# Performance work log

Hardware: AMD Instinct MI355X
Metric: run time of the kernel (lower is better)

## Reference

```python
import jax, jax.numpy as jnp
import numpy as np

EMBED_DIM = 768
NUM_HEADS = 12
HEAD_DIM = EMBED_DIM // NUM_HEADS
SCALE = HEAD_DIM ** -0.5


def setup_inputs() -> dict:
    key = jax.random.key(0)
    ks = jax.random.split(key, 9)
    B, S, D = 2, 2048, EMBED_DIM
    init = 1.0 / np.sqrt(D)  # ~ nn.Linear default uniform scale
    x = jax.random.normal(ks[0], (B, S, D), dtype=jnp.float32)
    Wq = jax.random.uniform(ks[1], (D, D), jnp.float32, -init, init)
    bq = jax.random.uniform(ks[2], (D,), jnp.float32, -init, init)
    Wk = jax.random.uniform(ks[3], (D, D), jnp.float32, -init, init)
    bk = jax.random.uniform(ks[4], (D,), jnp.float32, -init, init)
    Wv = jax.random.uniform(ks[5], (D, D), jnp.float32, -init, init)
    bv = jax.random.uniform(ks[6], (D,), jnp.float32, -init, init)
    Wo = jax.random.uniform(ks[7], (D, D), jnp.float32, -init, init)
    bo = jax.random.uniform(ks[8], (D,), jnp.float32, -init, init)
    return {"x": x, "Wq": Wq, "bq": bq, "Wk": Wk, "bk": bk,
            "Wv": Wv, "bv": bv, "Wo": Wo, "bo": bo}


def reference(x, Wq, bq, Wk, bk, Wv, bv, Wo, bo):
    B, S, D = x.shape
    H, Dh = NUM_HEADS, HEAD_DIM
    # projections; weights stored as (in, out) so x @ W == torch Linear with W.T
    q = (x @ Wq + bq).reshape(B, S, H, Dh).transpose(0, 2, 1, 3)  # [B,H,S,Dh]
    k = (x @ Wk + bk).reshape(B, S, H, Dh).transpose(0, 2, 1, 3)
    v = (x @ Wv + bv).reshape(B, S, H, Dh).transpose(0, 2, 1, 3)
    scores = jnp.einsum("bhqd,bhkd->bhqk", q, k) * SCALE        # [B,H,S,S]
    weights = jax.nn.softmax(scores, axis=-1)
    out = jnp.einsum("bhqk,bhkd->bhqd", weights, v)              # [B,H,S,Dh]
    out = out.transpose(0, 2, 1, 3).reshape(B, S, D)
    return out @ Wo + bo
```

## Files before the change

### kernel.cpp

```cpp
#include <hip/hip_runtime.h>
#include <math.h>

#define BB 2
#define SS 2048
#define DDIM 768
#define HH 12
#define DH 64
#define NROWS (BB*SS)
#define NQT2 (SS/128)
#define NSPLIT 4

typedef _Float16 f16;
typedef _Float16 half2v __attribute__((ext_vector_type(2)));
typedef __fp16 fp16x2 __attribute__((ext_vector_type(2)));
typedef _Float16 half4 __attribute__((ext_vector_type(4)));
typedef _Float16 half8 __attribute__((ext_vector_type(8)));
typedef float f32x4 __attribute__((ext_vector_type(4)));
typedef float f32x16 __attribute__((ext_vector_type(16)));
typedef unsigned int u32;
typedef unsigned int u32x4v __attribute__((ext_vector_type(4)));

__device__ __forceinline__ half2v cvt_pk_f16(float a, float b) {
    fp16x2 t = __builtin_amdgcn_cvt_pkrtz(a, b);
    return __builtin_bit_cast(half2v, t);
}

#define MFMA16(a,b,c) __builtin_amdgcn_mfma_f32_16x16x32_f16((a),(b),(c),0,0,0)
#define MFMA32(a,b,c) __builtin_amdgcn_mfma_f32_32x32x16_f16((a),(b),(c),0,0,0)
#define QSCALE (0.125f * 1.44269504088896f)
#define M_STATIC 10.0f

__device__ __forceinline__ int swz(int row, int chunk16) {
    return row*128 + ((chunk16 ^ (row & 7)) << 4);
}

__global__ __launch_bounds__(256) void prep_w(const float* __restrict__ Wq, const float* __restrict__ Wk,
                                              const float* __restrict__ Wv, const float* __restrict__ Wo,
                                              f16* __restrict__ Wt)
{
    const int z = blockIdx.z;
    const float* W = z==0 ? Wq : (z==1 ? Wk : (z==2 ? Wv : Wo));
    f16* out = Wt + (size_t)z * DDIM * DDIM;

    __shared__ float tile[64][65];
    const int t = threadIdx.x;
    const int k0 = blockIdx.x*64, n0 = blockIdx.y*64;

    const int kr = t >> 2, nc = (t & 3) * 16;
    #pragma unroll
    for (int i = 0; i < 4; ++i) {
        float4 v = *(const float4*)&W[(size_t)(k0+kr)*DDIM + n0 + nc + i*4];
        tile[kr][nc+i*4+0] = v.x; tile[kr][nc+i*4+1] = v.y;
        tile[kr][nc+i*4+2] = v.z; tile[kr][nc+i*4+3] = v.w;
    }
    __syncthreads();
    const int nr = t >> 2, kc = (t & 3) * 16;
    half8 h0, h1;
    #pragma unroll
    for (int j = 0; j < 8; ++j) {
        h0[j] = (f16)tile[kc + j][nr];
        h1[j] = (f16)tile[kc + 8 + j][nr];
    }
    *(half8*)&out[(size_t)(n0+nr)*DDIM + k0 + kc]     = h0;
    *(half8*)&out[(size_t)(n0+nr)*DDIM + k0 + kc + 8] = h1;
}

__global__ __launch_bounds__(256) void proj_qkv(const float* __restrict__ x, const f16* __restrict__ Wt,
        const float* __restrict__ bq, const float* __restrict__ bk, const float* __restrict__ bv,
        f16* __restrict__ qb, f16* __restrict__ kb2, f16* __restrict__ vtb)
{
    const int z = blockIdx.z;
    const f16* Wz = Wt + (size_t)z * DDIM * DDIM;
    const float* bias = z==0 ? bq : (z==1 ? bk : bv);
    const float qscale = (z==0) ? QSCALE : 1.0f;

    __shared__ __align__(16) unsigned char lds[64*1024];

    const int tid = threadIdx.x;
    const int l = tid & 63, w = tid >> 6;
    const int g = l >> 4, qi = l & 15;
    const int wm = w >> 1, wn = w & 1;
    const int m0 = blockIdx.x * 128, n0 = blockIdx.y * 128;

    f32x4 acc[4][4];
    #pragma unroll
    for (int i=0;i<4;i++)
        #pragma unroll
        for (int j=0;j<4;j++) { f32x4 zv = {0.f,0.f,0.f,0.f}; acc[i][j] = zv; }

    half8 sa[4], sb[4];

#define GLOAD(t) { \
        _Pragma("unroll") \
        for (int i = 0; i < 4; ++i) { \
            int c = i*256 + tid, row = c >> 3, kc = c & 7; \
            const float* xp = &x[(size_t)(m0+row)*DDIM + (t)*64 + kc*8]; \
            float4 a0 = *(const float4*)xp; \
            float4 a1 = *(const float4*)(xp + 4); \
            half8 hv = {(f16)a0.x,(f16)a0.y,(f16)a0.z,(f16)a0.w, \
                        (f16)a1.x,(f16)a1.y,(f16)a1.z,(f16)a1.w}; \
            sa[i] = hv; \
            sb[i] = *(const half8*)&Wz[(size_t)(n0+row)*DDIM + (t)*64 + kc*8]; \
        } }

#define GWRT(bufi) { \
        unsigned char* As_ = lds + (bufi)*32768; \
        unsigned char* Bs_ = As_ + 16384; \
        _Pragma("unroll") \
        for (int i = 0; i < 4; ++i) { \
            int c = i*256 + tid, row = c >> 3, kc = c & 7; \
            *(half8*)(As_ + swz(row, kc)) = sa[i]; \
            *(half8*)(Bs_ + swz(row, kc)) = sb[i]; \
        } }

    GLOAD(0); GWRT(0);
    __syncthreads();

    for (int t = 0; t < 12; ++t) {
        const int cur = t & 1;
        if (t < 11) GLOAD(t+1);

        const unsigned char* As = lds + cur*32768;
        const unsigned char* Bs = As + 16384;

        half8 af[4][2], bf[4][2];
        #pragma unroll
        for (int mt = 0; mt < 4; ++mt) {
            int row = wm*64 + mt*16 + qi;
            #pragma unroll
            for (int kh = 0; kh < 2; ++kh)
                af[mt][kh] = *(const half8*)(As + swz(row, kh*4 + g));
        }
        #pragma unroll
        for (int nt = 0; nt < 4; ++nt) {
            int row = wn*64 + nt*16 + qi;
            #pragma unroll
            for (int kh = 0; kh < 2; ++kh)
                bf[nt][kh] = *(const half8*)(Bs + swz(row, kh*4 + g));
        }
        __builtin_amdgcn_s_setprio(1);
        #pragma unroll
        for (int mt = 0; mt < 4; ++mt)
            #pragma unroll
            for (int nt = 0; nt < 4; ++nt) {
                acc[mt][nt] = MFMA16(af[mt][0], bf[nt][0], acc[mt][nt]);
                acc[mt][nt] = MFMA16(af[mt][1], bf[nt][1], acc[mt][nt]);
            }
        __builtin_amdgcn_s_setprio(0);

        if (t < 11) GWRT(cur^1);
        __syncthreads();
    }

    if (z == 2) {
        #pragma unroll
        for (int mt = 0; mt < 4; ++mt)
            #pragma unroll
            for (int nt = 0; nt < 4; ++nt) {
                int m = m0 + wm*64 + mt*16 + g*4;
                int n = n0 + wn*64 + nt*16 + qi;
                int b = m >> 11, s = m & 2047;
                int h = n >> 6,  d = n & 63;
                float bs = bias[n];
                half4 o4 = {(f16)(acc[mt][nt][0] + bs), (f16)(acc[mt][nt][1] + bs),
                            (f16)(acc[mt][nt][2] + bs), (f16)(acc[mt][nt][3] + bs)};
                *(half4*)&vtb[(((size_t)(b*HH + h))*DH + d)*SS + s] = o4;
            }
    } else {
        f16* out = (z == 0) ? qb : kb2;
        #pragma unroll
        for (int mt = 0; mt < 4; ++mt)
            #pragma unroll
            for (int nt = 0; nt < 4; ++nt)
                #pragma unroll
                for (int r = 0; r < 4; ++r) {
                    int m = m0 + wm*64 + mt*16 + g*4 + r;
                    int n = n0 + wn*64 + nt*16 + qi;
                    float v = (acc[mt][nt][r] + bias[n]) * qscale;
                    int b = m >> 11, s = m & 2047;
                    int h = n >> 6,  d = n & 63;
                    out[(((size_t)(b*HH + h))*SS + s)*DH + d] = (f16)v;
                }
    }
#undef GLOAD
#undef GWRT
}

__global__ __launch_bounds__(256) void attn_mfma(
        const f16* __restrict__ qbuf, const f16* __restrict__ kbuf,
        const f16* __restrict__ vtbuf, f16* __restrict__ pO, float* __restrict__ mlb)
{
    __shared__ __align__(16) unsigned char lds[32*1024];

    const int tid = threadIdx.x;
    const int l = tid & 63, w = tid >> 6;
    const int q31 = l & 31, hl = l >> 5;
    const int qt = blockIdx.x, h = blockIdx.y;
    const int b = blockIdx.z >> 2, kq = blockIdx.z & 3;
    const int q0 = qt * 128 + w * 32;
    const size_t base = ((size_t)(b * HH + h)) * SS * DH;
    const int key0 = kq * (SS/NSPLIT);
    const int pid = (b * HH + h) * NQT2 + qt;

    half8 qf[4];
    #pragma unroll
    for (int s = 0; s < 4; ++s)
        qf[s] = *(const half8*)&qbuf[base + (size_t)(q0 + q31)*DH + s*16 + hl*8];

    f32x16 oacc[2];
    #pragma unroll
    for (int dt = 0; dt < 2; ++dt)
        #pragma unroll
        for (int i = 0; i < 16; ++i) oacc[dt][i] = 0.f;
    float lsum = 0.f;
    f32x16 minit16;
    #pragma unroll
    for (int i = 0; i < 16; ++i) minit16[i] = -M_STATIC;

    half8 sk[2], svv[2];

#define LOADT(t) { \
        _Pragma("unroll") \
        for (int i = 0; i < 2; ++i) { \
            int c = i*256 + tid, row = c >> 3, col = c & 7; \
            sk[i]  = *(const half8*)&kbuf[base + (size_t)(key0 + (t)*64 + row)*DH + col*8]; \
            svv[i] = *(const half8*)&vtbuf[base + (size_t)row*SS + key0 + (t)*64 + col*8]; \
        } }

#define WRT(bufi) { \
        unsigned char* Kw_ = lds + (bufi)*16384; \
        unsigned char* Vw_ = Kw_ + 8192; \
        _Pragma("unroll") \
        for (int i = 0; i < 2; ++i) { \
            int c = i*256 + tid, row = c >> 3, col = c & 7; \
            *(half8*)(Kw_ + swz(row, col)) = sk[i]; \
            *(half8*)(Vw_ + swz(row, col)) = svv[i]; \
        } }

    LOADT(0); WRT(0);
    __syncthreads();

    for (int t = 0; t < 8; ++t) {
        const int cur = t & 1;
        if (t < 7) LOADT(t+1);

        const unsigned char* Kb = lds + cur*16384;
        const unsigned char* Vb = Kb + 8192;

        half8 kA[2][4];
        #pragma unroll
        for (int mt = 0; mt < 2; ++mt)
            #pragma unroll
            for (int s = 0; s < 4; ++s)
                kA[mt][s] = *(const half8*)(Kb + swz(mt*32 + q31, 2*s + hl));
        half8 vA[2][4];
        #pragma unroll
        for (int dt = 0; dt < 2; ++dt)
            #pragma unroll
            for (int ks = 0; ks < 4; ++ks)
                vA[dt][ks] = *(const half8*)(Vb + swz(dt*32 + q31, 2*ks + hl));

        half2v ph[16];
        #pragma unroll
        for (int mt = 0; mt < 2; ++mt) {
            __builtin_amdgcn_s_setprio(1);
            f32x16 sv = minit16;
            #pragma unroll
            for (int s = 0; s < 4; ++s)
                sv = MFMA32(kA[mt][s], qf[s], sv);
            __builtin_amdgcn_s_setprio(0);
            #pragma unroll
            for (int r = 0; r < 16; r += 2)
                ph[mt*8 + (r>>1)] = cvt_pk_f16(exp2f(sv[r]), exp2f(sv[r+1]));
        }

        {
            half2v t01 = (ph[0]+ph[1]) + (ph[2]+ph[3]);
            half2v t23 = (ph[4]+ph[5]) + (ph[6]+ph[7]);
            half2v t45 = (ph[8]+ph[9]) + (ph[10]+ph[11]);
            half2v t67 = (ph[12]+ph[13]) + (ph[14]+ph[15]);
            half2v tt = (t01+t23) + (t45+t67);
            float rs = (float)tt[0] + (float)tt[1];
            rs += __shfl_xor(rs, 32);
            lsum += rs;
        }

        half8 pf[4];
        #pragma unroll
        for (int ks = 0; ks < 4; ++ks) {
            u32 x0 = __builtin_bit_cast(u32, ph[4*ks + 0]);
            u32 x2 = __builtin_bit_cast(u32, ph[4*ks + 2]);
            asm volatile("v_permlane32_swap_b32 %0, %1" : "+v"(x0), "+v"(x2));
            u32 x1 = __builtin_bit_cast(u32, ph[4*ks + 1]);
            u32 x3 = __builtin_bit_cast(u32, ph[4*ks + 3]);
            asm volatile("v_permlane32_swap_b32 %0, %1" : "+v"(x1), "+v"(x3));
            u32x4v tv = {x0, x1, x2, x3};
            pf[ks] = __builtin_bit_cast(half8, tv);
        }

        __builtin_amdgcn_s_setprio(1);
        #pragma unroll
        for (int dt = 0; dt < 2; ++dt)
            #pragma unroll
            for (int ks = 0; ks < 4; ++ks)
                oacc[dt] = MFMA32(vA[dt][ks], pf[ks], oacc[dt]);
        __builtin_amdgcn_s_setprio(0);

        if (t < 7) WRT(cur^1);
        __syncthreads();
    }

    f16* po = pO + ((size_t)pid*NSPLIT + kq) * (128*64);
    float* mlp = mlb + ((size_t)pid*NSPLIT + kq) * 128;
    const int qw = w*32 + q31;
    const float inv = 1.0f / lsum;
    #pragma unroll
    for (int dt = 0; dt < 2; ++dt)
        #pragma unroll
        for (int g2 = 0; g2 < 4; ++g2) {
            half4 o4 = {(f16)(oacc[dt][g2*4+0]*inv), (f16)(oacc[dt][g2*4+1]*inv),
                        (f16)(oacc[dt][g2*4+2]*inv), (f16)(oacc[dt][g2*4+3]*inv)};
            *(half4*)&po[qw*64 + dt*32 + g2*8 + hl*4] = o4;
        }
    if (hl == 0) mlp[qw] = lsum;
#undef LOADT
#undef WRT
}

__global__ __launch_bounds__(256) void attn_combine(
        const f16* __restrict__ pO, const float* __restrict__ mlb, f16* __restrict__ ob)
{
    const int gr = blockIdx.x*64 + (threadIdx.x >> 2);
    const int dg = (threadIdx.x & 3) << 4;
    const int bh = gr >> 11, s = gr & 2047;
    const int qt = s >> 7, qr = s & 127;
    const int pid = bh * NQT2 + qt;

    float lv[NSPLIT], lt = 0.f;
    #pragma unroll
    for (int i = 0; i < NSPLIT; ++i) {
        lv[i] = mlb[((size_t)pid*NSPLIT + i)*128 + qr];
        lt += lv[i];
    }
    const float inv = 1.0f / lt;

    float a0[8] = {}, a1[8] = {};
    #pragma unroll
    for (int i = 0; i < NSPLIT; ++i) {
        const f16* Oi = pO + ((size_t)pid*NSPLIT + i)*(128*64) + qr*64 + dg;
        half8 x0 = *(const half8*)Oi;
        half8 x1 = *(const half8*)(Oi + 8);
        float wi = lv[i] * inv;
        #pragma unroll
        for (int j = 0; j < 8; ++j) {
            a0[j] += wi * (float)x0[j];
            a1[j] += wi * (float)x1[j];
        }
    }
    half8 r0, r1;
    #pragma unroll
    for (int j = 0; j < 8; ++j) { r0[j] = (f16)a0[j]; r1[j] = (f16)a1[j]; }
    f16* dst = &ob[((size_t)bh*SS + s)*DH + dg];
    *(half8*)dst = r0;
    *(half8*)(dst + 8) = r1;
}

__global__ __launch_bounds__(256) void proj_out(const f16* __restrict__ obuf, const f16* __restrict__ Wt,
                                                const float* __restrict__ bo, float* __restrict__ out)
{
    const f16* Wz = Wt + (size_t)3 * DDIM * DDIM;

    __shared__ __align__(16) unsigned char lds[64*1024];

    const int tid = threadIdx.x;
    const int l = tid & 63, w = tid >> 6;
    const int g = l >> 4, qi = l & 15;
    const int wm = w >> 1, wn = w & 1;
    const int m0 = blockIdx.x * 128, n0 = blockIdx.y * 128;

    f32x4 acc[4][4];
    #pragma unroll
    for (int i=0;i<4;i++)
        #pragma unroll
        for (int j=0;j<4;j++) { f32x4 zv = {0.f,0.f,0.f,0.f}; acc[i][j] = zv; }

    half8 sa[4], sb[4];

#define GLOAD(t) { \
        _Pragma("unroll") \
        for (int i = 0; i < 4; ++i) { \
            int c = i*256 + tid, row = c >> 3, kc = c & 7; \
            int m = m0 + row, bb_ = m >> 11, ss_ = m & 2047; \
            sa[i] = *(const half8*)&obuf[(((size_t)(bb_*HH + (t)))*SS + ss_)*DH + kc*8]; \
            sb[i] = *(const half8*)&Wz[(size_t)(n0+row)*DDIM + (t)*64 + kc*8]; \
        } }

#define GWRT(bufi) { \
        unsigned char* As_ = lds + (bufi)*32768; \
        unsigned char* Bs_ = As_ + 16384; \
        _Pragma("unroll") \
        for (int i = 0; i < 4; ++i) { \
            int c = i*256 + tid, row = c >> 3, kc = c & 7; \
            *(half8*)(As_ + swz(row, kc)) = sa[i]; \
            *(half8*)(Bs_ + swz(row, kc)) = sb[i]; \
        } }

    GLOAD(0); GWRT(0);
    __syncthreads();

    for (int t = 0; t < 12; ++t) {
        const int cur = t & 1;
        if (t < 11) GLOAD(t+1);

        const unsigned char* As = lds + cur*32768;
        const unsigned char* Bs = As + 16384;

        half8 af[4][2], bf[4][2];
        #pragma unroll
        for (int mt = 0; mt < 4; ++mt) {
            int row = wm*64 + mt*16 + qi;
            #pragma unroll
            for (int kh = 0; kh < 2; ++kh)
                af[mt][kh] = *(const half8*)(As + swz(row, kh*4 + g));
        }
        #pragma unroll
        for (int nt = 0; nt < 4; ++nt) {
            int row = wn*64 + nt*16 + qi;
            #pragma unroll
            for (int kh = 0; kh < 2; ++kh)
                bf[nt][kh] = *(const half8*)(Bs + swz(row, kh*4 + g));
        }
        __builtin_amdgcn_s_setprio(1);
        #pragma unroll
        for (int mt = 0; mt < 4; ++mt)
            #pragma unroll
            for (int nt = 0; nt < 4; ++nt) {
                acc[mt][nt] = MFMA16(af[mt][0], bf[nt][0], acc[mt][nt]);
                acc[mt][nt] = MFMA16(af[mt][1], bf[nt][1], acc[mt][nt]);
            }
        __builtin_amdgcn_s_setprio(0);

        if (t < 11) GWRT(cur^1);
        __syncthreads();
    }

    #pragma unroll
    for (int mt = 0; mt < 4; ++mt)
        #pragma unroll
        for (int nt = 0; nt < 4; ++nt)
            #pragma unroll
            for (int r = 0; r < 4; ++r) {
                int m = m0 + wm*64 + mt*16 + g*4 + r;
                int n = n0 + wn*64 + nt*16 + qi;
                out[(size_t)m*DDIM + n] = acc[mt][nt][r] + bo[n];
            }
#undef GLOAD
#undef GWRT
}

extern "C" void kernel_launch(void* const* d_in, const int* in_sizes, int n_in,
                              void* d_out, int out_size, void* d_ws, size_t ws_size,
                              hipStream_t stream)
{
    const float* x  = (const float*)d_in[0];
    const float* Wq = (const float*)d_in[1];
    const float* bq = (const float*)d_in[2];
    const float* Wk = (const float*)d_in[3];
    const float* bk = (const float*)d_in[4];
    const float* Wv = (const float*)d_in[5];
    const float* bv = (const float*)d_in[6];
    const float* Wo = (const float*)d_in[7];
    const float* bo = (const float*)d_in[8];

    char* ws = (char*)d_ws;
    const size_t WT_B  = (size_t)4 * DDIM * DDIM * 2;
    const size_t HB_B  = (size_t)BB * HH * SS * DH * 2;
    const size_t PO_B  = (size_t)BB * HH * NQT2 * NSPLIT * 128 * 64 * 2;
    const size_t ML_B  = (size_t)BB * HH * NQT2 * NSPLIT * 128 * 4;

    f16* Wt = (f16*)ws;
    f16* qb = (f16*)(ws + WT_B);
    f16* kb = (f16*)(ws + WT_B + HB_B);
    f16* vt = (f16*)(ws + WT_B + 2*HB_B);
    f16* pO = (f16*)(ws + WT_B + 3*HB_B);
    float* mlb = (float*)(ws + WT_B + 3*HB_B + PO_B);
    f16* ob = (f16*)(ws + WT_B + 3*HB_B + PO_B + ML_B);

    prep_w<<<dim3(DDIM/64, DDIM/64, 4), 256, 0, stream>>>(Wq, Wk, Wv, Wo, Wt);
    proj_qkv<<<dim3(NROWS/128, DDIM/128, 3), 256, 0, stream>>>(x, Wt, bq, bk, bv, qb, kb, vt);
    attn_mfma<<<dim3(NQT2, HH, BB*NSPLIT), 256, 0, stream>>>(qb, kb, vt, pO, mlb);
    attn_combine<<<dim3(BB*HH*SS/64), 256, 0, stream>>>(pO, mlb, ob);
    proj_out<<<dim3(NROWS/128, DDIM/128), 256, 0, stream>>>(ob, Wt, bo, (float*)d_out);
}
```

Measured before the change: 118.6 us.

## Shrink projection GEMM tiles to 64x128 with single-buffered LDS

```diff
diff --git a/kernel.cpp b/kernel.cpp
--- a/kernel.cpp
+++ b/kernel.cpp
@@ -74,25 +74,27 @@
     const float* bias = z==0 ? bq : (z==1 ? bk : bv);
     const float qscale = (z==0) ? QSCALE : 1.0f;
 
-    __shared__ __align__(16) unsigned char lds[64*1024];
+    __shared__ __align__(16) unsigned char lds[24*1024];
+    unsigned char* As = lds;
+    unsigned char* Bs = lds + 8192;
 
     const int tid = threadIdx.x;
     const int l = tid & 63, w = tid >> 6;
     const int g = l >> 4, qi = l & 15;
     const int wm = w >> 1, wn = w & 1;
-    const int m0 = blockIdx.x * 128, n0 = blockIdx.y * 128;
-
-    f32x4 acc[4][4];
-    #pragma unroll
-    for (int i=0;i<4;i++)
+    const int m0 = blockIdx.x * 64, n0 = blockIdx.y * 128;
+
+    f32x4 acc[2][4];
+    #pragma unroll
+    for (int i=0;i<2;i++)
         #pragma unroll
         for (int j=0;j<4;j++) { f32x4 zv = {0.f,0.f,0.f,0.f}; acc[i][j] = zv; }
 
-    half8 sa[4], sb[4];
+    half8 sa[2], sb[4];
 
 #define GLOAD(t) { \
         _Pragma("unroll") \
-        for (int i = 0; i < 4; ++i) { \
+        for (int i = 0; i < 2; ++i) { \
             int c = i*256 + tid, row = c >> 3, kc = c & 7; \
             const float* xp = &x[(size_t)(m0+row)*DDIM + (t)*64 + kc*8]; \
             float4 a0 = *(const float4*)xp; \
@@ -100,33 +102,35 @@
             half8 hv = {(f16)a0.x,(f16)a0.y,(f16)a0.z,(f16)a0.w, \
                         (f16)a1.x,(f16)a1.y,(f16)a1.z,(f16)a1.w}; \
             sa[i] = hv; \
+        } \
+        _Pragma("unroll") \
+        for (int i = 0; i < 4; ++i) { \
+            int c = i*256 + tid, row = c >> 3, kc = c & 7; \
             sb[i] = *(const half8*)&Wz[(size_t)(n0+row)*DDIM + (t)*64 + kc*8]; \
         } }
 
-#define GWRT(bufi) { \
-        unsigned char* As_ = lds + (bufi)*32768; \
-        unsigned char* Bs_ = As_ + 16384; \
+#define GWRT { \
+        _Pragma("unroll") \
+        for (int i = 0; i < 2; ++i) { \
+            int c = i*256 + tid, row = c >> 3, kc = c & 7; \
+            *(half8*)(As + swz(row, kc)) = sa[i]; \
+        } \
         _Pragma("unroll") \
         for (int i = 0; i < 4; ++i) { \
             int c = i*256 + tid, row = c >> 3, kc = c & 7; \
-            *(half8*)(As_ + swz(row, kc)) = sa[i]; \
-            *(half8*)(Bs_ + swz(row, kc)) = sb[i]; \
+            *(half8*)(Bs + swz(row, kc)) = sb[i]; \
         } }
 
-    GLOAD(0); GWRT(0);
+    GLOAD(0); GWRT;
     __syncthreads();
 
     for (int t = 0; t < 12; ++t) {
-        const int cur = t & 1;
         if (t < 11) GLOAD(t+1);
 
-        const unsigned char* As = lds + cur*32768;
-        const unsigned char* Bs = As + 16384;
-
-        half8 af[4][2], bf[4][2];
-        #pragma unroll
-        for (int mt = 0; mt < 4; ++mt) {
-            int row = wm*64 + mt*16 + qi;
+        half8 af[2][2], bf[4][2];
+        #pragma unroll
+        for (int mt = 0; mt < 2; ++mt) {
+            int row = wm*32 + mt*16 + qi;
             #pragma unroll
             for (int kh = 0; kh < 2; ++kh)
                 af[mt][kh] = *(const half8*)(As + swz(row, kh*4 + g));
@@ -140,7 +144,7 @@
         }
         __builtin_amdgcn_s_setprio(1);
         #pragma unroll
-        for (int mt = 0; mt < 4; ++mt)
+        for (int mt = 0; mt < 2; ++mt)
             #pragma unroll
             for (int nt = 0; nt < 4; ++nt) {
                 acc[mt][nt] = MFMA16(af[mt][0], bf[nt][0], acc[mt][nt]);
@@ -148,16 +152,19 @@
             }
         __builtin_amdgcn_s_setprio(0);
 
-        if (t < 11) GWRT(cur^1);
-        __syncthreads();
+        if (t < 11) {
+            __syncthreads();
+            GWRT;
+            __syncthreads();
+        }
     }
 
     if (z == 2) {
         #pragma unroll
-        for (int mt = 0; mt < 4; ++mt)
+        for (int mt = 0; mt < 2; ++mt)
             #pragma unroll
             for (int nt = 0; nt < 4; ++nt) {
-                int m = m0 + wm*64 + mt*16 + g*4;
+                int m = m0 + wm*32 + mt*16 + g*4;
                 int n = n0 + wn*64 + nt*16 + qi;
                 int b = m >> 11, s = m & 2047;
                 int h = n >> 6,  d = n & 63;
@@ -169,12 +176,12 @@
     } else {
         f16* out = (z == 0) ? qb : kb2;
         #pragma unroll
-        for (int mt = 0; mt < 4; ++mt)
+        for (int mt = 0; mt < 2; ++mt)
             #pragma unroll
             for (int nt = 0; nt < 4; ++nt)
                 #pragma unroll
                 for (int r = 0; r < 4; ++r) {
-                    int m = m0 + wm*64 + mt*16 + g*4 + r;
+                    int m = m0 + wm*32 + mt*16 + g*4 + r;
                     int n = n0 + wn*64 + nt*16 + qi;
                     float v = (acc[mt][nt][r] + bias[n]) * qscale;
                     int b = m >> 11, s = m & 2047;
@@ -370,55 +377,59 @@
 {
     const f16* Wz = Wt + (size_t)3 * DDIM * DDIM;
 
-    __shared__ __align__(16) unsigned char lds[64*1024];
+    __shared__ __align__(16) unsigned char lds[24*1024];
+    unsigned char* As = lds;
+    unsigned char* Bs = lds + 8192;
 
     const int tid = threadIdx.x;
     const int l = tid & 63, w = tid >> 6;
     const int g = l >> 4, qi = l & 15;
     const int wm = w >> 1, wn = w & 1;
-    const int m0 = blockIdx.x * 128, n0 = blockIdx.y * 128;
-
-    f32x4 acc[4][4];
-    #pragma unroll
-    for (int i=0;i<4;i++)
+    const int m0 = blockIdx.x * 64, n0 = blockIdx.y * 128;
+
+    f32x4 acc[2][4];
+    #pragma unroll
+    for (int i=0;i<2;i++)
         #pragma unroll
         for (int j=0;j<4;j++) { f32x4 zv = {0.f,0.f,0.f,0.f}; acc[i][j] = zv; }
 
-    half8 sa[4], sb[4];
+    half8 sa[2], sb[4];
 
 #define GLOAD(t) { \
         _Pragma("unroll") \
-        for (int i = 0; i < 4; ++i) { \
+        for (int i = 0; i < 2; ++i) { \
             int c = i*256 + tid, row = c >> 3, kc = c & 7; \
             int m = m0 + row, bb_ = m >> 11, ss_ = m & 2047; \
             sa[i] = *(const half8*)&obuf[(((size_t)(bb_*HH + (t)))*SS + ss_)*DH + kc*8]; \
+        } \
+        _Pragma("unroll") \
+        for (int i = 0; i < 4; ++i) { \
+            int c = i*256 + tid, row = c >> 3, kc = c & 7; \
             sb[i] = *(const half8*)&Wz[(size_t)(n0+row)*DDIM + (t)*64 + kc*8]; \
         } }
 
-#define GWRT(bufi) { \
-        unsigned char* As_ = lds + (bufi)*32768; \
-        unsigned char* Bs_ = As_ + 16384; \
+#define GWRT { \
+        _Pragma("unroll") \
+        for (int i = 0; i < 2; ++i) { \
+            int c = i*256 + tid, row = c >> 3, kc = c & 7; \
+            *(half8*)(As + swz(row, kc)) = sa[i]; \
+        } \
         _Pragma("unroll") \
         for (int i = 0; i < 4; ++i) { \
             int c = i*256 + tid, row = c >> 3, kc = c & 7; \
-            *(half8*)(As_ + swz(row, kc)) = sa[i]; \
-            *(half8*)(Bs_ + swz(row, kc)) = sb[i]; \
+            *(half8*)(Bs + swz(row, kc)) = sb[i]; \
         } }
 
-    GLOAD(0); GWRT(0);
+    GLOAD(0); GWRT;
     __syncthreads();
 
     for (int t = 0; t < 12; ++t) {
-        const int cur = t & 1;
         if (t < 11) GLOAD(t+1);
 
-        const unsigned char* As = lds + cur*32768;
-        const unsigned char* Bs = As + 16384;
-
-        half8 af[4][2], bf[4][2];
-        #pragma unroll
-        for (int mt = 0; mt < 4; ++mt) {
-            int row = wm*64 + mt*16 + qi;
+        half8 af[2][2], bf[4][2];
+        #pragma unroll
+        for (int mt = 0; mt < 2; ++mt) {
+            int row = wm*32 + mt*16 + qi;
             #pragma unroll
             for (int kh = 0; kh < 2; ++kh)
                 af[mt][kh] = *(const half8*)(As + swz(row, kh*4 + g));
@@ -432,7 +443,7 @@
         }
         __builtin_amdgcn_s_setprio(1);
         #pragma unroll
-        for (int mt = 0; mt < 4; ++mt)
+        for (int mt = 0; mt < 2; ++mt)
             #pragma unroll
             for (int nt = 0; nt < 4; ++nt) {
                 acc[mt][nt] = MFMA16(af[mt][0], bf[nt][0], acc[mt][nt]);
@@ -440,17 +451,20 @@
             }
         __builtin_amdgcn_s_setprio(0);
 
-        if (t < 11) GWRT(cur^1);
-        __syncthreads();
-    }
-
-    #pragma unroll
-    for (int mt = 0; mt < 4; ++mt)
+        if (t < 11) {
+            __syncthreads();
+            GWRT;
+            __syncthreads();
+        }
+    }
+
+    #pragma unroll
+    for (int mt = 0; mt < 2; ++mt)
         #pragma unroll
         for (int nt = 0; nt < 4; ++nt)
             #pragma unroll
             for (int r = 0; r < 4; ++r) {
-                int m = m0 + wm*64 + mt*16 + g*4 + r;
+                int m = m0 + wm*32 + mt*16 + g*4 + r;
                 int n = n0 + wn*64 + nt*16 + qi;
                 out[(size_t)m*DDIM + n] = acc[mt][nt][r] + bo[n];
             }
@@ -487,8 +501,8 @@
     f16* ob = (f16*)(ws + WT_B + 3*HB_B + PO_B + ML_B);
 
     prep_w<<<dim3(DDIM/64, DDIM/64, 4), 256, 0, stream>>>(Wq, Wk, Wv, Wo, Wt);
-    proj_qkv<<<dim3(NROWS/128, DDIM/128, 3), 256, 0, stream>>>(x, Wt, bq, bk, bv, qb, kb, vt);
+    proj_qkv<<<dim3(NROWS/64, DDIM/128, 3), 256, 0, stream>>>(x, Wt, bq, bk, bv, qb, kb, vt);
     attn_mfma<<<dim3(NQT2, HH, BB*NSPLIT), 256, 0, stream>>>(qb, kb, vt, pO, mlb);
     attn_combine<<<dim3(BB*HH*SS/64), 256, 0, stream>>>(pO, mlb, ob);
-    proj_out<<<dim3(NROWS/128, DDIM/128), 256, 0, stream>>>(ob, Wt, bo, (float*)d_out);
-}
+    proj_out<<<dim3(NROWS/64, DDIM/128), 256, 0, stream>>>(ob, Wt, bo, (float*)d_out);
+}
```

Result: no change. 116.7 us, median of 2 (-1.6%).
